# Performance work log

Hardware: AMD Instinct MI355X
Metric: run time of the kernel (lower is better)

Reference implementation:

```python
import jax, jax.numpy as jnp
import numpy as np

N_NODES = 50000
N_RAND_EDGES = 800000
IN_FEATS = 128
NUM_HEADS = 4
OUT_FEATS = 32
NEG_SLOPE = 0.2


def setup_inputs() -> dict:
    key = jax.random.key(0)
    k_feat, k_src, k_dst, k_w, k_al, k_ar, k_b = jax.random.split(key, 7)
    feat = jax.random.normal(k_feat, (N_NODES, IN_FEATS), dtype=jnp.float32)
    # random edges + self-loops so every node has in-degree >= 1 (DGL requirement)
    src_r = jax.random.randint(k_src, (N_RAND_EDGES,), 0, N_NODES)
    dst_r = jax.random.randint(k_dst, (N_RAND_EDGES,), 0, N_NODES)
    loops = jnp.arange(N_NODES, dtype=src_r.dtype)
    src = jnp.concatenate([src_r, loops]).astype(jnp.int64)
    dst = jnp.concatenate([dst_r, loops]).astype(jnp.int64)
    W = jax.random.normal(k_w, (NUM_HEADS * OUT_FEATS, IN_FEATS), dtype=jnp.float32) * 0.05
    attn_l = jax.random.normal(k_al, (1, NUM_HEADS, OUT_FEATS), dtype=jnp.float32) * 0.1
    attn_r = jax.random.normal(k_ar, (1, NUM_HEADS, OUT_FEATS), dtype=jnp.float32) * 0.1
    bias = jnp.zeros((NUM_HEADS * OUT_FEATS,), dtype=jnp.float32)
    return {"feat": feat, "src": src, "dst": dst, "W": W,
            "attn_l": attn_l, "attn_r": attn_r, "bias": bias}


def _gat_forward(feat, src, dst, W, attn_l, attn_r, bias):
    n = feat.shape[0]
    # shared projection: in homogeneous path feat_src2 = feat_dst2 = fc(h)
    ft = (feat @ W.T).reshape(n, NUM_HEADS, OUT_FEATS)       # [N,H,D]
    el = jnp.sum(ft * attn_l, axis=-1)                        # [N,H]
    er = jnp.sum(ft * attn_r, axis=-1)                        # [N,H]
    e = el[src] + er[dst]                                     # [E,H]
    e = jnp.where(e > 0, e, NEG_SLOPE * e)                    # leaky_relu
    # edge softmax per destination node (numerically stable)
    m = jax.ops.segment_max(e, dst, num_segments=n)           # [N,H]
    ex = jnp.exp(e - m[dst])
    s = jax.ops.segment_sum(ex, dst, num_segments=n)          # [N,H]
    a = ex / s[dst]                                           # [E,H]
    # u_mul_e -> sum : attention-weighted aggregation
    msg1 = ft[src] * a[:, :, None]                            # [E,H,D]
    initial_ft = jax.ops.segment_sum(msg1, dst, num_segments=n)
    # u_mul_v -> sum : elementwise src*dst product aggregation
    msg2 = ft[src] * ft[dst]                                  # [E,H,D]
    add_ft = jax.ops.segment_sum(msg2, dst, num_segments=n)
    rst = initial_ft + add_ft + bias.reshape(1, NUM_HEADS, OUT_FEATS)
    return rst


def reference(feat, src, dst, W, attn_l, attn_r, bias):
    return _gat_forward(feat, src, dst, W, attn_l, attn_r, bias)
```

## Files before the change

kernel.cpp:

```cpp
#include <hip/hip_runtime.h>
#include <hip/hip_bf16.h>

#define IN_FEATS 128
#define HD 128
#define NEG_SLOPE 0.2f
#define LDR 128
#define CAP 64
#define BINW 256
#define SEGC 64
#define SC 256
#define GPB 8
#define NPG 32
#define GM 64
#define LDA 136

typedef short s8v __attribute__((ext_vector_type(8)));
typedef float f4v __attribute__((ext_vector_type(4)));
typedef float f2v __attribute__((ext_vector_type(2)));

static __device__ __forceinline__ unsigned short f2bf(float f) {
    unsigned int u = __float_as_uint(f);
    unsigned int r = (u + 0x7FFFu + ((u >> 16) & 1u)) >> 16;
    return (unsigned short)r;
}

static __device__ __forceinline__ void stage_W(unsigned short (*Wb)[LDA],
                                               const float* __restrict__ W) {
    const float4* W4 = (const float4*)W;
    for (int i = threadIdx.x; i < 4096; i += 256) {
        int r = i >> 5, q = i & 31;
        float4 w = W4[i];
        ushort4 o;
        o.x = f2bf(w.x); o.y = f2bf(w.y); o.z = f2bf(w.z); o.w = f2bf(w.w);
        *(ushort4*)&Wb[r][q * 4] = o;
    }
}

static __device__ __forceinline__ void gemm_tile(
        unsigned short (*Wb)[LDA], unsigned short (*Ab)[LDA],
        const float* __restrict__ feat, const float* __restrict__ attn_l,
        const float* __restrict__ attn_r, unsigned short* __restrict__ ftb,
        float* __restrict__ el, float* __restrict__ er, int N, int rbase) {
    const int tid  = threadIdx.x;
    const int wave = tid >> 6;
    const int lane = tid & 63;
    const int m    = lane & 15;
    const int quad = lane >> 4;

    const float4* F4 = (const float4*)feat;
    for (int i = tid; i < 2048; i += 256) {
        int r = i >> 5, q = i & 31;
        int gr = rbase + r;
        float4 v = (gr < N) ? F4[(size_t)gr * 32 + q]
                            : make_float4(0.f, 0.f, 0.f, 0.f);
        ushort4 o;
        o.x = f2bf(v.x); o.y = f2bf(v.y); o.z = f2bf(v.z); o.w = f2bf(v.w);
        *(ushort4*)&Ab[r][q * 4] = o;
    }
    __syncthreads();

    f4v acc[8];
#pragma unroll
    for (int t = 0; t < 8; ++t) acc[t] = (f4v){0.f, 0.f, 0.f, 0.f};

    const int arow = wave * 16 + m;
#pragma unroll
    for (int k0 = 0; k0 < 4; ++k0) {
        s8v a = *(const s8v*)&Ab[arow][k0 * 32 + quad * 8];
#pragma unroll
        for (int t = 0; t < 8; ++t) {
            s8v b = *(const s8v*)&Wb[t * 16 + m][k0 * 32 + quad * 8];
            acc[t] = __builtin_amdgcn_mfma_f32_16x16x32_bf16(a, b, acc[t], 0, 0, 0);
        }
    }

#pragma unroll
    for (int reg = 0; reg < 4; ++reg) {
        int gr = rbase + wave * 16 + quad * 4 + reg;
        if (gr < N) {
            unsigned short* dstrow = &ftb[(size_t)gr * LDR];
#pragma unroll
            for (int t = 0; t < 8; ++t)
                dstrow[t * 16 + m] = f2bf(acc[t][reg]);
        }
    }

    float al[8], ar[8];
#pragma unroll
    for (int t = 0; t < 8; ++t) {
        al[t] = attn_l[t * 16 + m];
        ar[t] = attn_r[t * 16 + m];
    }
#pragma unroll
    for (int h = 0; h < 4; ++h) {
#pragma unroll
        for (int reg = 0; reg < 4; ++reg) {
            float pl = acc[2 * h][reg] * al[2 * h] + acc[2 * h + 1][reg] * al[2 * h + 1];
            float pr = acc[2 * h][reg] * ar[2 * h] + acc[2 * h + 1][reg] * ar[2 * h + 1];
            pl += __shfl_xor(pl, 1); pr += __shfl_xor(pr, 1);
            pl += __shfl_xor(pl, 2); pr += __shfl_xor(pr, 2);
            pl += __shfl_xor(pl, 4); pr += __shfl_xor(pr, 4);
            pl += __shfl_xor(pl, 8); pr += __shfl_xor(pr, 8);
            if (m == 0) {
                int gr = rbase + wave * 16 + quad * 4 + reg;
                if (gr < N) {
                    el[gr * 4 + h] = pl;
                    er[gr * 4 + h] = pr;
                }
            }
        }
    }
}

__global__ __launch_bounds__(256) void scatter_gemm(
        const float* __restrict__ feat, const float* __restrict__ W,
        const float* __restrict__ attn_l, const float* __restrict__ attn_r,
        const int* __restrict__ src, const int* __restrict__ dst, int ER,
        unsigned int* __restrict__ binbuf, unsigned short* __restrict__ cntBB,
        unsigned short* __restrict__ ftb, float* __restrict__ el,
        float* __restrict__ er, int N, int nbins) {
    __shared__ __align__(16) char smem[52224];
    const int tid = threadIdx.x;
    const int bid = blockIdx.x;
    if (bid < SC) {
        int* lcnt = (int*)smem;
        lcnt[tid] = 0;
        __syncthreads();
        const int chunk = (ER + SC - 1) / SC;
        const int base = bid * chunk;
        const int end = min(base + chunk, ER);
        for (int i = base + tid; i < end; i += 256) {
            int d = dst[i];
            int s = src[i];
            int bin = d >> 8;
            int r = atomicAdd(&lcnt[bin], 1);
            if (r < SEGC)
                binbuf[((((unsigned int)bin << 8) + bid) << 6) + r] =
                    ((unsigned int)(d & 255) << 16) | (unsigned int)s;
        }
        __syncthreads();
        if (tid < nbins)
            cntBB[tid * 256 + bid] = (unsigned short)min(lcnt[tid], SEGC);
        return;
    }
    unsigned short (*Wb)[LDA] = (unsigned short (*)[LDA])smem;
    unsigned short (*Ab)[LDA] = (unsigned short (*)[LDA])(smem + 128 * LDA * 2);
    stage_W(Wb, W);
    gemm_tile(Wb, Ab, feat, attn_l, attn_r, ftb, el, er, N,
              (bid - SC) * GM);
}

__global__ __launch_bounds__(256) void bucket_agg(
        const unsigned int* __restrict__ binbuf, const unsigned short* __restrict__ cntBB,
        const unsigned short* __restrict__ ftb, const float* __restrict__ el,
        const float* __restrict__ er, const float* __restrict__ bias,
        float* __restrict__ out, int N, int nbins) {
    const int bin = blockIdx.x >> 3;
    const int g   = blockIdx.x & (GPB - 1);
    const int tid = threadIdx.x;

    __shared__ unsigned short lb[NPG * CAP];
    __shared__ int lcnt[NPG];
    __shared__ unsigned short cnts[256];

    if (tid < NPG) lcnt[tid] = 0;
    cnts[tid] = cntBB[bin * 256 + tid];
    __syncthreads();

    const int wave = tid >> 6;
    const int lane = tid & 63;

    for (int sg = 0; sg < 4; ++sg) {
        const int seg = (wave << 6) + (sg << 4) + (lane >> 2);
        const int c = cnts[seg];
        const unsigned int* sp = binbuf + ((((unsigned int)bin << 8) + seg) << 6);
        for (int j = lane & 3; j < c; j += 4) {
            unsigned int v = sp[j];
            int dl = (int)(v >> 16);
            if ((dl >> 5) == g) {
                int ln = dl & (NPG - 1);
                int pos = atomicAdd(&lcnt[ln], 1);
                if (pos < CAP) lb[(ln << 6) + pos] = (unsigned short)(v & 0xFFFFu);
            }
        }
    }
    __syncthreads();

    const int h  = lane >> 4;
    const int c0 = lane * 2;
    const unsigned int* ftbu = (const unsigned int*)ftb;

    for (int ln = wave; ln < NPG; ln += 4) {
        const int n = (bin << 8) + (g << 5) + ln;
        if (n >= N) break;

        const float ern = er[(n << 2) + h];
        unsigned int tn = ftbu[((unsigned int)n << 6) + lane];
        f2v ftn; ftn.x = __uint_as_float(tn << 16);
        ftn.y = __uint_as_float(tn & 0xFFFF0000u);

        float es = el[(n << 2) + h] + ern;
        es = fmaxf(es, NEG_SLOPE * es);
        const float xs = __expf(es);

        float sum = xs;
        f2v accA = xs * ftn;
        f2v accB = ftn;

        const int deg = min(lcnt[ln], CAP);
        const unsigned short* eb = &lb[ln << 6];

        int i = 0;
        for (; i + 4 <= deg; i += 4) {
            ushort4 s4 = *(const ushort4*)&eb[i];
            unsigned int sA = s4.x, sB = s4.y, sC = s4.z, sD = s4.w;
            float eA = el[(sA << 2) + h];
            float eB = el[(sB << 2) + h];
            float eC = el[(sC << 2) + h];
            float eD = el[(sD << 2) + h];
            unsigned int fA = ftbu[(sA << 6) + lane];
            unsigned int fB = ftbu[(sB << 6) + lane];
            unsigned int fC = ftbu[(sC << 6) + lane];
            unsigned int fD = ftbu[(sD << 6) + lane];
            eA += ern; eB += ern; eC += ern; eD += ern;
            eA = fmaxf(eA, NEG_SLOPE * eA);
            eB = fmaxf(eB, NEG_SLOPE * eB);
            eC = fmaxf(eC, NEG_SLOPE * eC);
            eD = fmaxf(eD, NEG_SLOPE * eD);
            float xA = __expf(eA), xB = __expf(eB);
            float xC = __expf(eC), xD = __expf(eD);
            f2v ffA; ffA.x = __uint_as_float(fA << 16); ffA.y = __uint_as_float(fA & 0xFFFF0000u);
            f2v ffB; ffB.x = __uint_as_float(fB << 16); ffB.y = __uint_as_float(fB & 0xFFFF0000u);
            f2v ffC; ffC.x = __uint_as_float(fC << 16); ffC.y = __uint_as_float(fC & 0xFFFF0000u);
            f2v ffD; ffD.x = __uint_as_float(fD << 16); ffD.y = __uint_as_float(fD & 0xFFFF0000u);
            sum += (xA + xB) + (xC + xD);
            accA += xA * ffA;
            accA += xB * ffB;
            accA += xC * ffC;
            accA += xD * ffD;
            accB += ffA + ffB;
            accB += ffC + ffD;
        }
        for (; i < deg; ++i) {
            unsigned int s = eb[i];
            float e = el[(s << 2) + h] + ern;
            e = fmaxf(e, NEG_SLOPE * e);
            float x = __expf(e);
            unsigned int f = ftbu[(s << 6) + lane];
            f2v ff; ff.x = __uint_as_float(f << 16); ff.y = __uint_as_float(f & 0xFFFF0000u);
            sum += x;
            accA += x * ff;
            accB += ff;
        }

        float inv = 1.f / sum;
        f2v o = accA * inv + ftn * accB;
        float2 ov;
        ov.x = o.x + bias[c0];
        ov.y = o.y + bias[c0 + 1];
        *(float2*)(out + (size_t)n * HD + c0) = ov;
    }
}

extern "C" void kernel_launch(void* const* d_in, const int* in_sizes, int n_in,
                              void* d_out, int out_size, void* d_ws, size_t ws_size,
                              hipStream_t stream) {
    const float* feat   = (const float*)d_in[0];
    const int*   src    = (const int*)d_in[1];
    const int*   dst    = (const int*)d_in[2];
    const float* W      = (const float*)d_in[3];
    const float* attn_l = (const float*)d_in[4];
    const float* attn_r = (const float*)d_in[5];
    const float* bias   = (const float*)d_in[6];

    const int N = in_sizes[0] / IN_FEATS;
    const int E = in_sizes[1];
    const int ER = E - N;
    const int nbins = (N + BINW - 1) / BINW;

    char* p = (char*)d_ws;
    auto alloc = [&](size_t bytes) {
        char* q = p;
        p += (bytes + 255) & ~(size_t)255;
        return q;
    };
    unsigned short* ftb  = (unsigned short*)alloc((size_t)N * LDR * 2);
    float* el      = (float*)alloc((size_t)N * 4 * 4);
    float* er      = (float*)alloc((size_t)N * 4 * 4);
    unsigned int* binbuf = (unsigned int*)alloc((size_t)nbins * 256 * SEGC * 4);
    unsigned short* cntBB = (unsigned short*)alloc((size_t)nbins * 256 * 2);

    const int gemm_blocks = (N + GM - 1) / GM;
    scatter_gemm<<<SC + gemm_blocks, 256, 0, stream>>>(
        feat, W, attn_l, attn_r, src, dst, ER, binbuf, cntBB, ftb, el, er,
        N, nbins);

    bucket_agg<<<nbins * GPB, 256, 0, stream>>>(binbuf, cntBB, ftb, el, er,
                                                bias, (float*)d_out, N, nbins);
}
```

Before: 158.9 us.

## Shrink GEMM LDS footprint by staging W in halves and loading A directly

The fused scatter/GEMM kernel drops the LDS staging of the feature tile. Each lane now loads its A fragment straight from global memory and converts it to bf16. W is staged into LDS in two 64-row halves, so shared memory falls from about 52KB to about 17KB and more blocks can be resident per CU, which should also help the scatter blocks. The cost is an extra sync and W restage per half, A fragments being reloaded from global memory for the second half, and less coalesced feature loads.

```diff
diff --git a/kernel.cpp b/kernel.cpp
--- a/kernel.cpp
+++ b/kernel.cpp
@@ -24,92 +24,13 @@
     return (unsigned short)r;
 }
 
-static __device__ __forceinline__ void stage_W(unsigned short (*Wb)[LDA],
-                                               const float* __restrict__ W) {
-    const float4* W4 = (const float4*)W;
-    for (int i = threadIdx.x; i < 4096; i += 256) {
-        int r = i >> 5, q = i & 31;
-        float4 w = W4[i];
-        ushort4 o;
-        o.x = f2bf(w.x); o.y = f2bf(w.y); o.z = f2bf(w.z); o.w = f2bf(w.w);
-        *(ushort4*)&Wb[r][q * 4] = o;
-    }
-}
-
-static __device__ __forceinline__ void gemm_tile(
-        unsigned short (*Wb)[LDA], unsigned short (*Ab)[LDA],
-        const float* __restrict__ feat, const float* __restrict__ attn_l,
-        const float* __restrict__ attn_r, unsigned short* __restrict__ ftb,
-        float* __restrict__ el, float* __restrict__ er, int N, int rbase) {
-    const int tid  = threadIdx.x;
-    const int wave = tid >> 6;
-    const int lane = tid & 63;
-    const int m    = lane & 15;
-    const int quad = lane >> 4;
-
-    const float4* F4 = (const float4*)feat;
-    for (int i = tid; i < 2048; i += 256) {
-        int r = i >> 5, q = i & 31;
-        int gr = rbase + r;
-        float4 v = (gr < N) ? F4[(size_t)gr * 32 + q]
-                            : make_float4(0.f, 0.f, 0.f, 0.f);
-        ushort4 o;
-        o.x = f2bf(v.x); o.y = f2bf(v.y); o.z = f2bf(v.z); o.w = f2bf(v.w);
-        *(ushort4*)&Ab[r][q * 4] = o;
-    }
-    __syncthreads();
-
-    f4v acc[8];
-#pragma unroll
-    for (int t = 0; t < 8; ++t) acc[t] = (f4v){0.f, 0.f, 0.f, 0.f};
-
-    const int arow = wave * 16 + m;
-#pragma unroll
-    for (int k0 = 0; k0 < 4; ++k0) {
-        s8v a = *(const s8v*)&Ab[arow][k0 * 32 + quad * 8];
-#pragma unroll
-        for (int t = 0; t < 8; ++t) {
-            s8v b = *(const s8v*)&Wb[t * 16 + m][k0 * 32 + quad * 8];
-            acc[t] = __builtin_amdgcn_mfma_f32_16x16x32_bf16(a, b, acc[t], 0, 0, 0);
-        }
-    }
-
-#pragma unroll
-    for (int reg = 0; reg < 4; ++reg) {
-        int gr = rbase + wave * 16 + quad * 4 + reg;
-        if (gr < N) {
-            unsigned short* dstrow = &ftb[(size_t)gr * LDR];
-#pragma unroll
-            for (int t = 0; t < 8; ++t)
-                dstrow[t * 16 + m] = f2bf(acc[t][reg]);
-        }
-    }
-
-    float al[8], ar[8];
-#pragma unroll
-    for (int t = 0; t < 8; ++t) {
-        al[t] = attn_l[t * 16 + m];
-        ar[t] = attn_r[t * 16 + m];
-    }
-#pragma unroll
-    for (int h = 0; h < 4; ++h) {
-#pragma unroll
-        for (int reg = 0; reg < 4; ++reg) {
-            float pl = acc[2 * h][reg] * al[2 * h] + acc[2 * h + 1][reg] * al[2 * h + 1];
-            float pr = acc[2 * h][reg] * ar[2 * h] + acc[2 * h + 1][reg] * ar[2 * h + 1];
-            pl += __shfl_xor(pl, 1); pr += __shfl_xor(pr, 1);
-            pl += __shfl_xor(pl, 2); pr += __shfl_xor(pr, 2);
-            pl += __shfl_xor(pl, 4); pr += __shfl_xor(pr, 4);
-            pl += __shfl_xor(pl, 8); pr += __shfl_xor(pr, 8);
-            if (m == 0) {
-                int gr = rbase + wave * 16 + quad * 4 + reg;
-                if (gr < N) {
-                    el[gr * 4 + h] = pl;
-                    er[gr * 4 + h] = pr;
-                }
-            }
-        }
-    }
+static __device__ __forceinline__ s8v pack8(float4 u0, float4 u1) {
+    s8v a;
+    a[0] = (short)f2bf(u0.x); a[1] = (short)f2bf(u0.y);
+    a[2] = (short)f2bf(u0.z); a[3] = (short)f2bf(u0.w);
+    a[4] = (short)f2bf(u1.x); a[5] = (short)f2bf(u1.y);
+    a[6] = (short)f2bf(u1.z); a[7] = (short)f2bf(u1.w);
+    return a;
 }
 
 __global__ __launch_bounds__(256) void scatter_gemm(
@@ -119,12 +40,15 @@
         unsigned int* __restrict__ binbuf, unsigned short* __restrict__ cntBB,
         unsigned short* __restrict__ ftb, float* __restrict__ el,
         float* __restrict__ er, int N, int nbins) {
-    __shared__ __align__(16) char smem[52224];
+    __shared__ __align__(16) union {
+        int lcnt[256];
+        unsigned short Wb[64][LDA];
+    } sm;
     const int tid = threadIdx.x;
     const int bid = blockIdx.x;
+
     if (bid < SC) {
-        int* lcnt = (int*)smem;
-        lcnt[tid] = 0;
+        sm.lcnt[tid] = 0;
         __syncthreads();
         const int chunk = (ER + SC - 1) / SC;
         const int base = bid * chunk;
@@ -133,21 +57,97 @@
             int d = dst[i];
             int s = src[i];
             int bin = d >> 8;
-            int r = atomicAdd(&lcnt[bin], 1);
+            int r = atomicAdd(&sm.lcnt[bin], 1);
             if (r < SEGC)
                 binbuf[((((unsigned int)bin << 8) + bid) << 6) + r] =
                     ((unsigned int)(d & 255) << 16) | (unsigned int)s;
         }
         __syncthreads();
         if (tid < nbins)
-            cntBB[tid * 256 + bid] = (unsigned short)min(lcnt[tid], SEGC);
+            cntBB[tid * 256 + bid] = (unsigned short)min(sm.lcnt[tid], SEGC);
         return;
     }
-    unsigned short (*Wb)[LDA] = (unsigned short (*)[LDA])smem;
-    unsigned short (*Ab)[LDA] = (unsigned short (*)[LDA])(smem + 128 * LDA * 2);
-    stage_W(Wb, W);
-    gemm_tile(Wb, Ab, feat, attn_l, attn_r, ftb, el, er, N,
-              (bid - SC) * GM);
+
+    const int wave  = tid >> 6;
+    const int lane  = tid & 63;
+    const int m     = lane & 15;
+    const int quad  = lane >> 4;
+    const int rbase = (bid - SC) * GM;
+    const int gr    = rbase + wave * 16 + m;
+    const float4* W4 = (const float4*)W;
+    const float4* Fr = (const float4*)(feat + (size_t)(gr < N ? gr : 0) * 128);
+    const bool arow_ok = (gr < N);
+
+    for (int half = 0; half < 2; ++half) {
+        __syncthreads();
+        for (int i = tid; i < 2048; i += 256) {
+            int r = i >> 5, q = i & 31;
+            float4 w = W4[(half * 64 + r) * 32 + q];
+            ushort4 o;
+            o.x = f2bf(w.x); o.y = f2bf(w.y); o.z = f2bf(w.z); o.w = f2bf(w.w);
+            *(ushort4*)&sm.Wb[r][q * 4] = o;
+        }
+        __syncthreads();
+
+        f4v acc[4];
+#pragma unroll
+        for (int tt = 0; tt < 4; ++tt) acc[tt] = (f4v){0.f, 0.f, 0.f, 0.f};
+
+#pragma unroll
+        for (int k0 = 0; k0 < 4; ++k0) {
+            s8v a;
+            if (arow_ok) {
+                float4 u0 = Fr[k0 * 8 + quad * 2];
+                float4 u1 = Fr[k0 * 8 + quad * 2 + 1];
+                a = pack8(u0, u1);
+            } else {
+                a = (s8v){0, 0, 0, 0, 0, 0, 0, 0};
+            }
+#pragma unroll
+            for (int tt = 0; tt < 4; ++tt) {
+                s8v b = *(const s8v*)&sm.Wb[tt * 16 + m][k0 * 32 + quad * 8];
+                acc[tt] = __builtin_amdgcn_mfma_f32_16x16x32_bf16(a, b, acc[tt], 0, 0, 0);
+            }
+        }
+
+#pragma unroll
+        for (int reg = 0; reg < 4; ++reg) {
+            int grr = rbase + wave * 16 + quad * 4 + reg;
+            if (grr < N) {
+                unsigned short* dstrow = &ftb[(size_t)grr * LDR];
+#pragma unroll
+                for (int tt = 0; tt < 4; ++tt)
+                    dstrow[(half * 4 + tt) * 16 + m] = f2bf(acc[tt][reg]);
+            }
+        }
+
+        float al[4], ar[4];
+#pragma unroll
+        for (int tt = 0; tt < 4; ++tt) {
+            al[tt] = attn_l[(half * 4 + tt) * 16 + m];
+            ar[tt] = attn_r[(half * 4 + tt) * 16 + m];
+        }
+#pragma unroll
+        for (int hh = 0; hh < 2; ++hh) {
+            int h = half * 2 + hh;
+#pragma unroll
+            for (int reg = 0; reg < 4; ++reg) {
+                float pl = acc[2 * hh][reg] * al[2 * hh] + acc[2 * hh + 1][reg] * al[2 * hh + 1];
+                float pr = acc[2 * hh][reg] * ar[2 * hh] + acc[2 * hh + 1][reg] * ar[2 * hh + 1];
+                pl += __shfl_xor(pl, 1); pr += __shfl_xor(pr, 1);
+                pl += __shfl_xor(pl, 2); pr += __shfl_xor(pr, 2);
+                pl += __shfl_xor(pl, 4); pr += __shfl_xor(pr, 4);
+                pl += __shfl_xor(pl, 8); pr += __shfl_xor(pr, 8);
+                if (m == 0) {
+                    int grr = rbase + wave * 16 + quad * 4 + reg;
+                    if (grr < N) {
+                        el[grr * 4 + h] = pl;
+                        er[grr * 4 + h] = pr;
+                    }
+                }
+            }
+        }
+    }
 }
 
 __global__ __launch_bounds__(256) void bucket_agg(
```

Result: no change. 160.4 us (+1.0%).
